# Kernel optimization log

Measured on AMD Instinct MI355X. Metric: run time of the kernel, lower is better.

## Reference

```python
import jax, jax.numpy as jnp
import numpy as np

DN = ('NCDHW', 'OIDHW', 'NCDHW')

def conv3d(x, w, b=None):
    y = jax.lax.conv_general_dilated(x, w, (1, 1, 1), 'SAME', dimension_numbers=DN)
    if b is not None:
        y = y + b[None, :, None, None, None]
    return y

def adaptive_conv(x, w):
    # x: [N,C,D,H,W], w: [N,27,D,H,W] (L1-normalized over channel dim)
    D, H, W = x.shape[2], x.shape[3], x.shape[4]
    p = jnp.pad(x, ((0, 0), (0, 0), (1, 1), (1, 1), (1, 1)))
    out = jnp.zeros_like(x)
    for i in range(3):
        for j in range(3):
            for k in range(3):
                t = i * 9 + j * 3 + k
                out = out + p[:, :, i:i + D, j:j + H, k:k + W] * w[:, t:t + 1]
    return out

def l1_normalize(w):
    # torch F.normalize(dim=1, p=1): denom clamped to 1e-12
    denom = jnp.maximum(jnp.sum(jnp.abs(w), axis=1, keepdims=True), 1e-12)
    return w / denom

def adaptive_block(x, w1, b1, w2, weights_src=None):
    src = x if weights_src is None else weights_src
    h = jax.nn.relu(conv3d(src, w1, b1))
    w = l1_normalize(conv3d(h, w2))  # [N,27,D,H,W]
    for _ in range(3):
        x = adaptive_conv(x, w)
    return x

def setup_inputs() -> dict:
    key = jax.random.key(0)
    ks = jax.random.split(key, 16)
    s = 0.05
    inp = {
        'x': jax.random.normal(ks[0], (1, 8, 128, 128, 128), dtype=jnp.float32),
        'ac1_w1': jax.random.normal(ks[1], (8, 8, 3, 3, 3), dtype=jnp.float32) * s,
        'ac1_b1': jnp.zeros((8,), dtype=jnp.float32),
        'ac1_w2': jax.random.normal(ks[2], (27, 8, 3, 3, 3), dtype=jnp.float32) * s,
        'ac2_w1': jax.random.normal(ks[3], (8, 8, 3, 3, 3), dtype=jnp.float32) * s,
        'ac2_b1': jnp.zeros((8,), dtype=jnp.float32),
        'ac2_w2': jax.random.normal(ks[4], (27, 8, 3, 3, 3), dtype=jnp.float32) * s,
        'ac3_w1': jax.random.normal(ks[5], (8, 8, 3, 3, 3), dtype=jnp.float32) * s,
        'ac3_b1': jnp.zeros((8,), dtype=jnp.float32),
        'ac3_w2': jax.random.normal(ks[6], (27, 8, 3, 3, 3), dtype=jnp.float32) * s,
        'mid_w': jax.random.normal(ks[7], (8, 8, 3, 3, 3), dtype=jnp.float32) * s,
        'mid_b': jnp.zeros((8,), dtype=jnp.float32),
        'out_w': jax.random.normal(ks[8], (1, 8, 3, 3, 3), dtype=jnp.float32) * s,
        'out_b': jnp.zeros((1,), dtype=jnp.float32),
    }
    return inp

def reference(x, ac1_w1, ac1_b1, ac1_w2, ac2_w1, ac2_b1, ac2_w2,
              ac3_w1, ac3_b1, ac3_w2, mid_w, mid_b, out_w, out_b):
    mid = adaptive_block(x, ac1_w1, ac1_b1, ac1_w2)
    mid = conv3d(mid, mid_w, mid_b)
    mid = adaptive_block(mid, ac2_w1, ac2_b1, ac2_w2)
    final = conv3d(mid, out_w, out_b)  # [N,1,D,H,W]
    final = adaptive_block(final, ac3_w1, ac3_b1, ac3_w2, weights_src=mid)
    return jnp.tanh(final)
```

## Files before the change

kernel.cpp:

```cpp
#include <hip/hip_runtime.h>
#include <math.h>

#define DSZ 128
#define VOX (DSZ*DSZ*DSZ)
#define PD  130

typedef _Float16 half8 __attribute__((ext_vector_type(8)));
typedef _Float16 half4 __attribute__((ext_vector_type(4)));
typedef _Float16 half2v __attribute__((ext_vector_type(2)));
typedef float float4v __attribute__((ext_vector_type(4)));


template<int CH>
__global__ __launch_bounds__(256) void zero_halo(_Float16* __restrict__ P)
{
    const int t = blockIdx.x * 256 + threadIdx.x;
    if (t >= PD * PD) return;
    const int zp = t / PD;
    const int yp = t - zp * PD;
    _Float16* row = P + (size_t)t * PD * CH;
    if (zp == 0 || zp == PD - 1 || yp == 0 || yp == PD - 1) {
        if (CH == 8) {
            half8 zz = {};
            for (int x = 0; x < PD; ++x) *(half8*)&row[x * 8] = zz;
        } else {
            for (int x = 0; x < PD; ++x) row[x] = (_Float16)0.0f;
        }
    } else {
        if (CH == 8) {
            half8 zz = {};
            *(half8*)&row[0] = zz;
            *(half8*)&row[(PD - 1) * 8] = zz;
        } else {
            row[0] = (_Float16)0.0f;
            row[PD - 1] = (_Float16)0.0f;
        }
    }
}

__global__ __launch_bounds__(256) void preformat(const float* __restrict__ w1a, const float* __restrict__ w1b,
                                                 const float* __restrict__ w1c, const float* __restrict__ outw,
                                                 const float* __restrict__ midw,
                                                 const float* __restrict__ w2a, const float* __restrict__ w2b,
                                                 const float* __restrict__ w2c, _Float16* __restrict__ WF)
{
    const int bid = blockIdx.x, tid = threadIdx.x;
    const float* src;
    _Float16* dst;
    int nelem, sz;
    if (bid < 3)       { src = bid == 0 ? w1a : bid == 1 ? w1b : w1c; dst = WF + bid * 3712; nelem = 8 * 216; sz = 16 * 29; }
    else if (bid == 3) { src = outw; dst = WF + 3 * 3712; nelem = 216;     sz = 16 * 29; }
    else if (bid == 4) { src = midw; dst = WF + 4 * 3712; nelem = 8 * 216; sz = 16 * 29; }
    else               { src = bid == 5 ? w2a : bid == 6 ? w2b : w2c; dst = WF + 5 * 3712 + (bid - 5) * 7424; nelem = 27 * 216; sz = 32 * 29; }
    for (int i = tid; i < sz; i += 256) ((half8*)dst)[i] = half8{};
    __syncthreads();
    for (int i = tid; i < nelem; i += 256) {
        const int oc = i / 216;
        const int rem = i - oc * 216;
        const int ic = rem / 27;
        const int tap = rem - ic * 27;
        dst[(oc * 29 + tap) * 8 + ic] = (_Float16)src[i];
    }
}

__global__ __launch_bounds__(256) void cast_hp(const float* __restrict__ in,
                                               _Float16* __restrict__ hp)
{
    const int idx = blockIdx.x * 256 + threadIdx.x;
    const int w = idx & 127;
    const int h = (idx >> 7) & 127;
    const int d = idx >> 14;
    half8 v;
    #pragma unroll
    for (int ic = 0; ic < 8; ++ic) v[ic] = (_Float16)in[(size_t)ic * VOX + idx];
    const int slot = ((d + 1) * PD + (h + 1)) * PD + (w + 1);
    *(half8*)&hp[(size_t)slot * 8] = v;
}

template<bool RELU>
__global__ __launch_bounds__(256) void conv8x8_mfma(const _Float16* __restrict__ DP,
                                                    const _Float16* __restrict__ WF,
                                                    const float* __restrict__ bias,
                                                    _Float16* __restrict__ HO)
{
    __shared__ _Float16 Wr[16 * 29 * 8];
    const int tid = threadIdx.x;
    for (int i = tid; i < 16 * 29; i += 256) ((half8*)Wr)[i] = ((const half8*)WF)[i];
    __syncthreads();

    const int b = ((blockIdx.x & 7) << 10) | (blockIdx.x >> 3);
    const int h0 = (b & 63) << 1;
    const int d  = b >> 6;
    const int lane = tid & 63;
    const int wv   = tid >> 6;
    const int col  = lane & 15;
    const int q    = lane >> 4;

    half8 af[7];
    #pragma unroll
    for (int c = 0; c < 7; ++c)
        af[c] = *(const half8*)&Wr[(col * 29 + (c * 4 + q)) * 8];

    const int base0 = ((d + 1) * PD + (h0 + 1)) * PD + 1 + wv * 32 + col;
    const _Float16* p[7];
    #pragma unroll
    for (int c = 0; c < 7; ++c) {
        const int tap = min(c * 4 + q, 26);
        const int dz = tap / 9, r9 = tap - dz * 9;
        const int dy = r9 / 3,  dx = r9 - dy * 3;
        p[c] = DP + (size_t)(base0 + ((dz - 1) * PD + (dy - 1)) * PD + (dx - 1)) * 8;
    }

    #pragma unroll
    for (int r = 0; r < 2; ++r) {
        #pragma unroll
        for (int t2 = 0; t2 < 2; ++t2) {
            float4v acc = {0.0f, 0.0f, 0.0f, 0.0f};
            #pragma unroll
            for (int c = 0; c < 7; ++c) {
                const half8 bv = *(const half8*)(p[c] + (r * PD + t2 * 16) * 8);
                acc = __builtin_amdgcn_mfma_f32_16x16x32_f16(af[c], bv, acc, 0, 0, 0);
            }
            if (q < 2) {
                const float4v bl = ((const float4v*)bias)[q];
                half4 hv;
                #pragma unroll
                for (int rr = 0; rr < 4; ++rr) {
                    float v = acc[rr] + bl[rr];
                    if (RELU) v = fmaxf(v, 0.0f);
                    hv[rr] = (_Float16)v;
                }
                *(half4*)&HO[(size_t)(base0 + r * PD + t2 * 16) * 8 + q * 4] = hv;
            }
        }
    }
}

__global__ __launch_bounds__(256) void conv8x1_mfma(const _Float16* __restrict__ DP,
                                                    const _Float16* __restrict__ WF,
                                                    const float* __restrict__ bias,
                                                    _Float16* __restrict__ F)
{
    __shared__ _Float16 Wr[16 * 29 * 8];
    const int tid = threadIdx.x;
    for (int i = tid; i < 16 * 29; i += 256) ((half8*)Wr)[i] = ((const half8*)WF)[i];
    __syncthreads();

    const int b = ((blockIdx.x & 7) << 10) | (blockIdx.x >> 3);
    const int h0 = (b & 63) << 1;
    const int d  = b >> 6;
    const int lane = tid & 63;
    const int wv   = tid >> 6;
    const int col  = lane & 15;
    const int q    = lane >> 4;

    half8 af[7];
    #pragma unroll
    for (int c = 0; c < 7; ++c)
        af[c] = *(const half8*)&Wr[(col * 29 + (c * 4 + q)) * 8];

    const int base0 = ((d + 1) * PD + (h0 + 1)) * PD + 1 + wv * 32 + col;
    const _Float16* p[7];
    #pragma unroll
    for (int c = 0; c < 7; ++c) {
        const int tap = min(c * 4 + q, 26);
        const int dz = tap / 9, r9 = tap - dz * 9;
        const int dy = r9 / 3,  dx = r9 - dy * 3;
        p[c] = DP + (size_t)(base0 + ((dz - 1) * PD + (dy - 1)) * PD + (dx - 1)) * 8;
    }

    const float b0 = bias[0];
    #pragma unroll
    for (int r = 0; r < 2; ++r) {
        #pragma unroll
        for (int t2 = 0; t2 < 2; ++t2) {
            float4v acc = {0.0f, 0.0f, 0.0f, 0.0f};
            #pragma unroll
            for (int c = 0; c < 7; ++c) {
                const half8 bv = *(const half8*)(p[c] + (r * PD + t2 * 16) * 8);
                acc = __builtin_amdgcn_mfma_f32_16x16x32_f16(af[c], bv, acc, 0, 0, 0);
            }
            if (q == 0)
                F[base0 + r * PD + t2 * 16] = (_Float16)(acc[0] + b0);
        }
    }
}

__global__ __launch_bounds__(256) void conv8x27n_mfma(const _Float16* __restrict__ HP,
                                                      const _Float16* __restrict__ WF,
                                                      _Float16* __restrict__ WB)
{
    __shared__ _Float16 Wr[32 * 29 * 8];
    __shared__ _Float16 T[3 * 6 * 130 * 8];
    const int tid = threadIdx.x;

    const int b = ((blockIdx.x & 7) << 9) | (blockIdx.x >> 3);
    const int h0 = (b & 31) << 2;
    const int d  = b >> 5;

    for (int i = tid; i < 32 * 29; i += 256) ((half8*)Wr)[i] = ((const half8*)WF)[i];
    for (int i = tid; i < 3 * 6 * 130; i += 256) {
        const int dz  = i / 780;
        const int rem = i - dz * 780;
        const int yy  = rem / 130;
        const int xs  = rem - yy * 130;
        ((half8*)T)[i] =
            *(const half8*)&HP[((size_t)((d + dz) * PD + (h0 + yy)) * PD + xs) * 8];
    }
    __syncthreads();

    const int lane = tid & 63;
    const int wv   = tid >> 6;
    const int col  = lane & 15;
    const int q    = lane >> 4;

    half8 af[2][7];
    #pragma unroll
    for (int t = 0; t < 2; ++t)
        #pragma unroll
        for (int c = 0; c < 7; ++c)
            af[t][c] = *(const half8*)&Wr[((t * 16 + col) * 29 + (c * 4 + q)) * 8];

    int lb[7];
    #pragma unroll
    for (int c = 0; c < 7; ++c) {
        const int tap = min(c * 4 + q, 26);
        const int dz = tap / 9, r9 = tap - dz * 9;
        const int dy = r9 / 3,  dx = r9 - dy * 3;
        lb[c] = ((dz * 6 + dy) * 130 + wv * 32 + col + dx) * 8;
    }

    #pragma unroll
    for (int r = 0; r < 4; ++r) {
        #pragma unroll
        for (int t2 = 0; t2 < 2; ++t2) {
            float4v acc0 = {0.0f, 0.0f, 0.0f, 0.0f};
            float4v acc1 = {0.0f, 0.0f, 0.0f, 0.0f};
            #pragma unroll
            for (int c = 0; c < 7; ++c) {
                const half8 bv = *(const half8*)&T[lb[c] + (r * 130 + t2 * 16) * 8];
                acc0 = __builtin_amdgcn_mfma_f32_16x16x32_f16(af[0][c], bv, acc0, 0, 0, 0);
                acc1 = __builtin_amdgcn_mfma_f32_16x16x32_f16(af[1][c], bv, acc1, 0, 0, 0);
            }

            float s = 0.0f;
            #pragma unroll
            for (int rr = 0; rr < 4; ++rr) {
                s += fabsf(acc0[rr]);
                if (16 + q * 4 + rr < 27) s += fabsf(acc1[rr]);
            }
            s += __shfl_xor(s, 16);
            s += __shfl_xor(s, 32);
            const float rcp = 1.0f / fmaxf(s, 1e-12f);

            const int vox = (d << 14) + ((h0 + r) << 7) + wv * 32 + t2 * 16 + col;
            const size_t base = (size_t)vox * 28;
            half4 o0, o1;
            #pragma unroll
            for (int rr = 0; rr < 4; ++rr) {
                o0[rr] = (_Float16)(acc0[rr] * rcp);
                o1[rr] = (_Float16)(acc1[rr] * rcp);
            }
            *(half4*)&WB[base + q * 4] = o0;
            if (q < 3)
                *(half4*)&WB[base + 16 + q * 4] = o1;
        }
    }
}

__global__ __launch_bounds__(256) void aconv8i(const _Float16* __restrict__ in,
                                               const _Float16* __restrict__ wb,
                                               _Float16* __restrict__ out)
{
    __shared__ _Float16 T[12 * 130 * 8];
    const int b = ((blockIdx.x & 7) << 10) | (blockIdx.x >> 3);
    const int h0 = (b & 63) << 1;
    const int d  = b >> 6;
    const int tid = threadIdx.x;

    for (int i = tid; i < 12 * 130; i += 256) {
        const int dz  = i / 520;
        const int rem = i - dz * 520;
        const int yy  = rem / 130;
        const int xs  = rem - yy * 130;
        ((half8*)T)[i] =
            *(const half8*)&in[((size_t)((d + dz) * PD + (h0 + yy)) * PD + xs) * 8];
    }
    __syncthreads();

    const int x   = tid & 127;
    const int ly  = tid >> 7;
    const int idx = b * 256 + tid;

    const size_t wbb = (size_t)idx * 28;
    half4 W[7];
    #pragma unroll
    for (int k = 0; k < 7; ++k) W[k] = *(const half4*)(wb + wbb + k * 4);

    half2v a4[4];
    #pragma unroll
    for (int j = 0; j < 4; ++j) a4[j] = half2v{};

    #pragma unroll
    for (int dz = 0; dz < 3; dz++) {
        #pragma unroll
        for (int dy = 0; dy < 3; dy++) {
            const _Float16* rp = &T[((dz * 4 + (ly + dy)) * 130 + (x + 1)) * 8];
            #pragma unroll
            for (int kw = 0; kw < 3; kw++) {
                const int tap = dz * 9 + dy * 3 + kw;
                const _Float16 wt = W[tap >> 2][tap & 3];
                half2v w2; w2[0] = wt; w2[1] = wt;
                const half8 hv = *(const half8*)(rp + (kw - 1) * 8);
                const half2v* h2 = (const half2v*)&hv;
                #pragma unroll
                for (int j = 0; j < 4; ++j)
                    a4[j] += h2[j] * w2;
            }
        }
    }

    const int s0 = ((d + 1) * PD + (h0 + ly + 1)) * PD + (x + 1);
    half8 o;
    #pragma unroll
    for (int j = 0; j < 4; ++j) { o[2 * j] = a4[j][0]; o[2 * j + 1] = a4[j][1]; }
    *(half8*)&out[(size_t)s0 * 8] = o;
}

template<bool TANH>
__global__ __launch_bounds__(256) void aconv1h(const _Float16* __restrict__ in,
                                               const _Float16* __restrict__ wb,
                                               _Float16* __restrict__ outh,
                                               float* __restrict__ outf)
{
    const int b = ((blockIdx.x & 7) << 10) | (blockIdx.x >> 3);
    const int idx = b * 256 + threadIdx.x;
    const int w = idx & 127;
    const int h = (idx >> 7) & 127;
    const int d = idx >> 14;

    const size_t wbb = (size_t)idx * 28;
    half4 W[7];
    #pragma unroll
    for (int k = 0; k < 7; ++k) W[k] = *(const half4*)(wb + wbb + k * 4);

    const int s0 = ((d + 1) * PD + (h + 1)) * PD + (w + 1);

    float acc = 0.0f;
    #pragma unroll
    for (int dz = 0; dz < 3; dz++) {
        #pragma unroll
        for (int dy = 0; dy < 3; dy++) {
            const _Float16* rp = in + s0 + ((dz - 1) * PD + (dy - 1)) * PD;
            #pragma unroll
            for (int kw = 0; kw < 3; kw++) {
                const int tap = dz * 9 + dy * 3 + kw;
                const _Float16 wt = W[tap >> 2][tap & 3];
                acc = fmaf((float)rp[kw - 1], (float)wt, acc);
            }
        }
    }

    if (TANH) outf[idx] = tanhf(acc);
    else      outh[s0] = (_Float16)acc;
}

extern "C" void kernel_launch(void* const* d_in, const int* in_sizes, int n_in,
                              void* d_out, int out_size, void* d_ws, size_t ws_size,
                              hipStream_t stream)
{
    const float* x      = (const float*)d_in[0];
    const float* ac1_w1 = (const float*)d_in[1];
    const float* ac1_b1 = (const float*)d_in[2];
    const float* ac1_w2 = (const float*)d_in[3];
    const float* ac2_w1 = (const float*)d_in[4];
    const float* ac2_b1 = (const float*)d_in[5];
    const float* ac2_w2 = (const float*)d_in[6];
    const float* ac3_w1 = (const float*)d_in[7];
    const float* ac3_b1 = (const float*)d_in[8];
    const float* ac3_w2 = (const float*)d_in[9];
    const float* mid_w  = (const float*)d_in[10];
    const float* mid_b  = (const float*)d_in[11];
    const float* out_w  = (const float*)d_in[12];
    const float* out_b  = (const float*)d_in[13];
    float* out = (float*)d_out;

    char* ws = (char*)d_ws;
    const size_t PS8 = (size_t)PD * PD * PD * 8 * 2;
    const size_t PS1 = (size_t)PD * PD * PD * 2;
    const size_t WBsz = (size_t)VOX * 28 * 2;
    _Float16* P0 = (_Float16*)(ws);
    _Float16* P1 = (_Float16*)(ws + PS8);
    _Float16* WB = (_Float16*)(ws + 2 * PS8);
    _Float16* F1 = (_Float16*)(ws + 2 * PS8 + WBsz);
    _Float16* G1 = (_Float16*)(ws + 2 * PS8 + WBsz + PS1);
    _Float16* F2 = (_Float16*)(ws + 2 * PS8 + WBsz + 2 * PS1);
    _Float16* WF = (_Float16*)(ws + 2 * PS8 + WBsz + 3 * PS1);
    _Float16* WF8_1  = WF;
    _Float16* WF8_2  = WF + 3712;
    _Float16* WF8_3  = WF + 7424;
    _Float16* WFo    = WF + 11136;
    _Float16* WFmid  = WF + 14848;
    _Float16* WF27_1 = WF + 18560;
    _Float16* WF27_2 = WF + 25984;
    _Float16* WF27_3 = WF + 33408;

    const dim3 blk(256);
    const dim3 gridT(VOX / 256);
    const dim3 gridM(VOX / 256);
    const dim3 gridM4(VOX / 512);
    const dim3 gridZ((PD * PD + 255) / 256);

    zero_halo<8><<<gridZ, blk, 0, stream>>>(P0);
    zero_halo<8><<<gridZ, blk, 0, stream>>>(P1);
    zero_halo<1><<<gridZ, blk, 0, stream>>>(F1);
    zero_halo<1><<<gridZ, blk, 0, stream>>>(G1);
    zero_halo<1><<<gridZ, blk, 0, stream>>>(F2);
    preformat<<<dim3(8), blk, 0, stream>>>(ac1_w1, ac2_w1, ac3_w1, out_w, mid_w,
                                           ac1_w2, ac2_w2, ac3_w2, WF);

    cast_hp<<<gridT, blk, 0, stream>>>(x, P0);
    conv8x8_mfma<true ><<<gridM, blk, 0, stream>>>(P0, WF8_1, ac1_b1, P1);
    conv8x27n_mfma<<<gridM4, blk, 0, stream>>>(P1, WF27_1, WB);
    aconv8i<<<gridT, blk, 0, stream>>>(P0, WB, P1);
    aconv8i<<<gridT, blk, 0, stream>>>(P1, WB, P0);
    aconv8i<<<gridT, blk, 0, stream>>>(P0, WB, P1);
    conv8x8_mfma<false><<<gridM, blk, 0, stream>>>(P1, WFmid, mid_b, P0);
    conv8x8_mfma<true ><<<gridM, blk, 0, stream>>>(P0, WF8_2, ac2_b1, P1);
    conv8x27n_mfma<<<gridM4, blk, 0, stream>>>(P1, WF27_2, WB);
    aconv8i<<<gridT, blk, 0, stream>>>(P0, WB, P1);
    aconv8i<<<gridT, blk, 0, stream>>>(P1, WB, P0);
    aconv8i<<<gridT, blk, 0, stream>>>(P0, WB, P1);
    conv8x8_mfma<true ><<<gridM, blk, 0, stream>>>(P1, WF8_3, ac3_b1, P0);
    conv8x27n_mfma<<<gridM4, blk, 0, stream>>>(P0, WF27_3, WB);
    conv8x1_mfma<<<gridM, blk, 0, stream>>>(P1, WFo, out_b, F1);
    aconv1h<false><<<gridT, blk, 0, stream>>>(F1, WB, G1, nullptr);
    aconv1h<false><<<gridT, blk, 0, stream>>>(G1, WB, F2, nullptr);
    aconv1h<true ><<<gridT, blk, 0, stream>>>(F2, WB, nullptr, out);
}
```

Before: 741.3 us.

## Stream depth slices through a rolling LDS ring in aconv8i

Each aconv8i block now covers 8 consecutive depth slices for a 2-row strip. It keeps a 4-slot shared-memory ring of padded z-planes, so each input plane is loaded once per block instead of three times, which cuts redundant global reads of the halo. The grid shrinks from 8192 to 1024 blocks, and each block pays an extra barrier per slice. Parallelism and latency hiding may drop because fewer blocks are resident and the stage/compute sequence is serial.

```diff
diff --git a/kernel.cpp b/kernel.cpp
--- a/kernel.cpp
+++ b/kernel.cpp
@@ -272,59 +272,69 @@
                                                const _Float16* __restrict__ wb,
                                                _Float16* __restrict__ out)
 {
-    __shared__ _Float16 T[12 * 130 * 8];
-    const int b = ((blockIdx.x & 7) << 10) | (blockIdx.x >> 3);
+    __shared__ _Float16 T[4][4 * 130 * 8];
+    const int b = ((blockIdx.x & 7) << 7) | (blockIdx.x >> 3);
     const int h0 = (b & 63) << 1;
-    const int d  = b >> 6;
+    const int d0 = (b >> 6) << 3;
     const int tid = threadIdx.x;
 
-    for (int i = tid; i < 12 * 130; i += 256) {
-        const int dz  = i / 520;
-        const int rem = i - dz * 520;
-        const int yy  = rem / 130;
-        const int xs  = rem - yy * 130;
-        ((half8*)T)[i] =
-            *(const half8*)&in[((size_t)((d + dz) * PD + (h0 + yy)) * PD + xs) * 8];
-    }
+    auto stage = [&](int z) {
+        const int slot = (z + 1) & 3;
+        for (int i = tid; i < 4 * 130; i += 256) {
+            const int yy = i / 130;
+            const int xs = i - yy * 130;
+            *(half8*)&T[slot][i * 8] =
+                *(const half8*)&in[((size_t)((z + 1) * PD + (h0 + yy)) * PD + xs) * 8];
+        }
+    };
+
+    stage(d0 - 1); stage(d0); stage(d0 + 1);
     __syncthreads();
 
-    const int x   = tid & 127;
-    const int ly  = tid >> 7;
-    const int idx = b * 256 + tid;
-
-    const size_t wbb = (size_t)idx * 28;
-    half4 W[7];
-    #pragma unroll
-    for (int k = 0; k < 7; ++k) W[k] = *(const half4*)(wb + wbb + k * 4);
-
-    half2v a4[4];
-    #pragma unroll
-    for (int j = 0; j < 4; ++j) a4[j] = half2v{};
-
-    #pragma unroll
-    for (int dz = 0; dz < 3; dz++) {
-        #pragma unroll
-        for (int dy = 0; dy < 3; dy++) {
-            const _Float16* rp = &T[((dz * 4 + (ly + dy)) * 130 + (x + 1)) * 8];
-            #pragma unroll
-            for (int kw = 0; kw < 3; kw++) {
-                const int tap = dz * 9 + dy * 3 + kw;
-                const _Float16 wt = W[tap >> 2][tap & 3];
-                half2v w2; w2[0] = wt; w2[1] = wt;
-                const half8 hv = *(const half8*)(rp + (kw - 1) * 8);
-                const half2v* h2 = (const half2v*)&hv;
+    const int x  = tid & 127;
+    const int ly = tid >> 7;
+
+    for (int z = d0; z < d0 + 8; ++z) {
+        if (z <= d0 + 6) stage(z + 2);
+
+        const int idx = (z << 14) + ((h0 + ly) << 7) + x;
+        const size_t wbb = (size_t)idx * 28;
+        half4 W[7];
+        #pragma unroll
+        for (int k = 0; k < 7; ++k) W[k] = *(const half4*)(wb + wbb + k * 4);
+
+        half2v a4[4];
+        #pragma unroll
+        for (int j = 0; j < 4; ++j) a4[j] = half2v{};
+
+        #pragma unroll
+        for (int dz = 0; dz < 3; dz++) {
+            const int slot = (z + dz) & 3;
+            #pragma unroll
+            for (int dy = 0; dy < 3; dy++) {
+                const _Float16* rp = &T[slot][((ly + dy) * 130 + (x + 1)) * 8];
                 #pragma unroll
-                for (int j = 0; j < 4; ++j)
-                    a4[j] += h2[j] * w2;
-            }
-        }
-    }
-
-    const int s0 = ((d + 1) * PD + (h0 + ly + 1)) * PD + (x + 1);
-    half8 o;
-    #pragma unroll
-    for (int j = 0; j < 4; ++j) { o[2 * j] = a4[j][0]; o[2 * j + 1] = a4[j][1]; }
-    *(half8*)&out[(size_t)s0 * 8] = o;
+                for (int kw = 0; kw < 3; kw++) {
+                    const int tap = dz * 9 + dy * 3 + kw;
+                    const _Float16 wt = W[tap >> 2][tap & 3];
+                    half2v w2; w2[0] = wt; w2[1] = wt;
+                    const half8 hv = *(const half8*)(rp + (kw - 1) * 8);
+                    const half2v* h2 = (const half2v*)&hv;
+                    #pragma unroll
+                    for (int j = 0; j < 4; ++j)
+                        a4[j] += h2[j] * w2;
+                }
+            }
+        }
+
+        const int s0 = ((z + 1) * PD + (h0 + ly + 1)) * PD + (x + 1);
+        half8 o;
+        #pragma unroll
+        for (int j = 0; j < 4; ++j) { o[2 * j] = a4[j][0]; o[2 * j + 1] = a4[j][1]; }
+        *(half8*)&out[(size_t)s0 * 8] = o;
+
+        __syncthreads();
+    }
 }
 
 template<bool TANH>
@@ -409,6 +419,7 @@
     const dim3 gridT(VOX / 256);
     const dim3 gridM(VOX / 256);
     const dim3 gridM4(VOX / 512);
+    const dim3 gridA(1024);
     const dim3 gridZ((PD * PD + 255) / 256);
 
     zero_halo<8><<<gridZ, blk, 0, stream>>>(P0);
@@ -422,15 +433,15 @@
     cast_hp<<<gridT, blk, 0, stream>>>(x, P0);
     conv8x8_mfma<true ><<<gridM, blk, 0, stream>>>(P0, WF8_1, ac1_b1, P1);
     conv8x27n_mfma<<<gridM4, blk, 0, stream>>>(P1, WF27_1, WB);
-    aconv8i<<<gridT, blk, 0, stream>>>(P0, WB, P1);
-    aconv8i<<<gridT, blk, 0, stream>>>(P1, WB, P0);
-    aconv8i<<<gridT, blk, 0, stream>>>(P0, WB, P1);
+    aconv8i<<<gridA, blk, 0, stream>>>(P0, WB, P1);
+    aconv8i<<<gridA, blk, 0, stream>>>(P1, WB, P0);
+    aconv8i<<<gridA, blk, 0, stream>>>(P0, WB, P1);
     conv8x8_mfma<false><<<gridM, blk, 0, stream>>>(P1, WFmid, mid_b, P0);
     conv8x8_mfma<true ><<<gridM, blk, 0, stream>>>(P0, WF8_2, ac2_b1, P1);
     conv8x27n_mfma<<<gridM4, blk, 0, stream>>>(P1, WF27_2, WB);
-    aconv8i<<<gridT, blk, 0, stream>>>(P0, WB, P1);
-    aconv8i<<<gridT, blk, 0, stream>>>(P1, WB, P0);
-    aconv8i<<<gridT, blk, 0, stream>>>(P0, WB, P1);
+    aconv8i<<<gridA, blk, 0, stream>>>(P0, WB, P1);
+    aconv8i<<<gridA, blk, 0, stream>>>(P1, WB, P0);
+    aconv8i<<<gridA, blk, 0, stream>>>(P0, WB, P1);
     conv8x8_mfma<true ><<<gridM, blk, 0, stream>>>(P1, WF8_3, ac3_b1, P0);
     conv8x27n_mfma<<<gridM4, blk, 0, stream>>>(P0, WF27_3, WB);
     conv8x1_mfma<<<gridM, blk, 0, stream>>>(P1, WFo, out_b, F1);
```

After: 728.2 us. Within noise of the previous version (-1.8%).
